# Kernel optimization log

Hardware: AMD Instinct MI355X
Metric: run time of the kernel (lower is better)

## Reference

```python
import jax, jax.numpy as jnp
import numpy as np

# Tier config (cumulative d_model [256,1024,2048], cumulative heads [4,12,24], d_k=64)
TIER_OWN = [256, 768, 1024]      # per-tier own hidden dims
HEAD_OUT = [256, 512, 768]       # n_heads_per_tier[i] * d_k
NHS = [4, 8, 12]
DKS = [64, 64, 64]
RANK = 8
IN_OFF = np.cumsum([0] + TIER_OWN)    # [0,256,1024,2048]
OUT_OFF = np.cumsum([0] + HEAD_OUT)   # [0,256,768,1536]


def _block_ut_weight(key, in_dims, out_dims):
    """Full (sum_in, sum_out) matrix with lower-triangular blocks zeroed."""
    io = np.cumsum([0] + list(in_dims))
    oo = np.cumsum([0] + list(out_dims))
    n = len(in_dims)
    mask = np.zeros((io[-1], oo[-1]), dtype=np.float32)
    for i in range(n):
        for j in range(i, n):
            mask[io[i]:io[i + 1], oo[j]:oo[j + 1]] = 1.0
    W = jax.random.normal(key, (io[-1], oo[-1]), dtype=jnp.float32) * 0.02
    return W * jnp.asarray(mask)


def setup_inputs() -> dict:
    key = jax.random.key(0)
    ks = jax.random.split(key, 16)
    B, T, D = 4, 1024, 2048
    x = jax.random.normal(ks[0], (B, T, D), dtype=jnp.float32)
    W_Q = _block_ut_weight(ks[1], TIER_OWN, HEAD_OUT)
    W_K = _block_ut_weight(ks[2], TIER_OWN, HEAD_OUT)
    W_V = _block_ut_weight(ks[3], TIER_OWN, HEAD_OUT)
    W_O = _block_ut_weight(ks[4], HEAD_OUT, TIER_OWN)
    # feedback for tiers 0 and 1 (tier 2 has no higher tiers)
    hi0 = TIER_OWN[1] + TIER_OWN[2]  # 1792
    hi1 = TIER_OWN[2]                # 1024
    FK0 = jax.random.normal(ks[5], (hi0, NHS[0] * RANK), dtype=jnp.float32) * 0.02
    PK0 = jax.random.normal(ks[6], (NHS[0], RANK, DKS[0]), dtype=jnp.float32) * 0.01
    FV0 = jax.random.normal(ks[7], (hi0, NHS[0] * RANK), dtype=jnp.float32) * 0.02
    PV0 = jax.random.normal(ks[8], (NHS[0], RANK, DKS[0]), dtype=jnp.float32) * 0.01
    FK1 = jax.random.normal(ks[9], (hi1, NHS[1] * RANK), dtype=jnp.float32) * 0.02
    PK1 = jax.random.normal(ks[10], (NHS[1], RANK, DKS[1]), dtype=jnp.float32) * 0.01
    FV1 = jax.random.normal(ks[11], (hi1, NHS[1] * RANK), dtype=jnp.float32) * 0.02
    PV1 = jax.random.normal(ks[12], (NHS[1], RANK, DKS[1]), dtype=jnp.float32) * 0.01
    return dict(x=x, W_Q=W_Q, W_K=W_K, W_V=W_V, W_O=W_O,
                FK0=FK0, PK0=PK0, FV0=FV0, PV0=PV0,
                FK1=FK1, PK1=PK1, FV1=FV1, PV1=PV1)


def _forward(x, W_Q, W_K, W_V, W_O, FK0, PK0, FV0, PV0, FK1, PK1, FV1, PV1):
    B, T, _ = x.shape
    Q_all = x @ W_Q
    K_all = x @ W_K
    V_all = x @ W_V
    causal = jnp.tril(jnp.ones((T, T), dtype=bool))
    fb = {0: (FK0, PK0, FV0, PV0), 1: (FK1, PK1, FV1, PV1)}
    head_outs = []
    for tier in range(3):
        nh, dk = NHS[tier], DKS[tier]
        dim = nh * dk
        o = int(OUT_OFF[tier])
        Q = Q_all[..., o:o + dim]
        K = K_all[..., o:o + dim]
        V = V_all[..., o:o + dim]
        if tier in fb:
            Fk, Pk, Fv, Pv = fb[tier]
            h_hi = x[..., int(IN_OFF[tier + 1]):]  # higher tiers' hidden
            c_k = (h_hi @ Fk).reshape(B, T, nh, RANK)
            K = K + jnp.einsum('bthr,hrd->bthd', c_k, Pk).reshape(B, T, dim)
            c_v = (h_hi @ Fv).reshape(B, T, nh, RANK)
            V = V + jnp.einsum('bthr,hrd->bthd', c_v, Pv).reshape(B, T, dim)
        Qh = Q.reshape(B, T, nh, dk).transpose(0, 2, 1, 3)
        Kh = K.reshape(B, T, nh, dk).transpose(0, 2, 1, 3)
        Vh = V.reshape(B, T, nh, dk).transpose(0, 2, 1, 3)
        scores = jnp.einsum('bhqd,bhkd->bhqk', Qh, Kh) / jnp.sqrt(jnp.float32(dk))
        scores = jnp.where(causal, scores, jnp.float32(-1e30))
        attn = jax.nn.softmax(scores, axis=-1)
        out = jnp.einsum('bhqk,bhkd->bhqd', attn, Vh)
        head_outs.append(out.transpose(0, 2, 1, 3).reshape(B, T, dim))
    return jnp.concatenate(head_outs, axis=-1) @ W_O


def reference(x, W_Q, W_K, W_V, W_O, FK0, PK0, FV0, PV0, FK1, PK1, FV1, PV1):
    return _forward(x, W_Q, W_K, W_V, W_O, FK0, PK0, FV0, PV0, FK1, PK1, FV1, PV1)
```

## Files before the change

kernel.cpp:

```cpp
#include <hip/hip_runtime.h>


typedef short bf16x8 __attribute__((ext_vector_type(8)));
typedef float floatx4 __attribute__((ext_vector_type(4)));

__device__ __forceinline__ unsigned short f2bf(float f) {
  unsigned u = __builtin_bit_cast(unsigned, f);
  u += 0x7fffu + ((u >> 16) & 1u);
  return (unsigned short)(u >> 16);
}

__device__ __forceinline__ void gload_lds16(const unsigned short* g, unsigned short* l) {
  __builtin_amdgcn_global_load_lds((const __attribute__((address_space(1))) unsigned int*)g,
                                   (__attribute__((address_space(3))) unsigned int*)l, 16, 0, 0);
}

__global__ __launch_bounds__(256) void k_prep(
    const float* __restrict__ x, unsigned short* __restrict__ X16,
    const float* __restrict__ WQ, const float* __restrict__ WK, const float* __restrict__ WV,
    const float* __restrict__ FK0, const float* __restrict__ PK0,
    const float* __restrict__ FV0, const float* __restrict__ PV0,
    const float* __restrict__ FK1, const float* __restrict__ PK1,
    const float* __restrict__ FV1, const float* __restrict__ PV1,
    unsigned short* __restrict__ WTQKV,
    const float* __restrict__ WO, unsigned short* __restrict__ WTO) {
  __shared__ float tile[32][33];
  __shared__ float Fs[32][9];
  __shared__ float Ps[8][32];
  const int bid = blockIdx.x;
  const int tid = threadIdx.x;
  if (bid < 8192) {
    int i = bid * 256 + tid;
    float4 v = ((const float4*)x)[i];
    union { unsigned short u[4]; uint2 v2; } o;
    o.u[0] = f2bf(v.x); o.u[1] = f2bf(v.y); o.u[2] = f2bf(v.z); o.u[3] = f2bf(v.w);
    ((uint2*)X16)[i] = o.v2;
    return;
  }
  const int tx = tid & 31, ty = tid >> 5;
  if (bid < 17408) {
    int t = bid - 8192;
    int k0 = (t & 63) * 32, n0 = (t >> 6) * 32;
    const float* src; int nboff;
    if (n0 < 1536)      { src = WQ; nboff = n0; }
    else if (n0 < 3072) { src = WK; nboff = n0 - 1536; }
    else                { src = WV; nboff = n0 - 3072; }
#pragma unroll
    for (int j = 0; j < 4; ++j) {
      int kk = ty + j * 8;
      tile[kk][tx] = src[(size_t)(k0 + kk) * 1536 + nboff + tx];
    }
    int corrsel = 0; const float* Fsrc = nullptr; const float* Psrc = nullptr;
    int h = 0, d0 = 0, fs = 0, koff = 0;
    if (n0 >= 1536) {
      bool isK = (n0 < 3072);
      int np0 = isK ? (n0 - 1536) : (n0 - 3072);
      if (np0 < 256) {
        if (k0 >= 256) { corrsel = 1; Fsrc = isK ? FK0 : FV0; Psrc = isK ? PK0 : PV0;
                         h = np0 >> 6; d0 = np0 & 63; fs = 32; koff = k0 - 256; }
      } else if (np0 < 768) {
        if (k0 >= 1024) { corrsel = 1; Fsrc = isK ? FK1 : FV1; Psrc = isK ? PK1 : PV1;
                          h = (np0 - 256) >> 6; d0 = (np0 - 256) & 63; fs = 64; koff = k0 - 1024; }
      }
    }
    if (corrsel) {
      Fs[tid >> 3][tid & 7] = Fsrc[(size_t)(koff + (tid >> 3)) * fs + h * 8 + (tid & 7)];
      Ps[tid >> 5][tid & 31] = Psrc[h * 512 + (tid >> 5) * 64 + d0 + (tid & 31)];
    }
    __syncthreads();
#pragma unroll
    for (int j = 0; j < 4; ++j) {
      int nn = ty + j * 8;
      float v = tile[tx][nn];
      if (corrsel) {
        float c = 0.f;
#pragma unroll
        for (int r = 0; r < 8; ++r) c += Fs[tx][r] * Ps[r][nn];
        v += c;
      }
      WTQKV[(size_t)(n0 + nn) * 2048 + k0 + tx] = f2bf(v);
    }
  } else {
    int t = bid - 17408;
    int k0 = (t % 48) * 32, n0 = (t / 48) * 32;
#pragma unroll
    for (int j = 0; j < 4; ++j)
      tile[ty + j * 8][tx] = WO[(size_t)(k0 + ty + j * 8) * 2048 + n0 + tx];
    __syncthreads();
#pragma unroll
    for (int j = 0; j < 4; ++j)
      WTO[(size_t)(n0 + ty + j * 8) * 1536 + k0 + tx] = f2bf(tile[tx][ty + j * 8]);
  }
}

__device__ __forceinline__ int lds_off(int row, int kq) {
  int L = row >> 1;
  return L * 64 + ((((row & 1) << 2) | kq) ^ (L & 7)) * 8;
}

__global__ __launch_bounds__(512) void k_gemm1(const unsigned short* __restrict__ A,
                                               const unsigned short* __restrict__ Bt,
                                               unsigned short* __restrict__ C) {
  __shared__ unsigned short Ls[3][2][8192];
  const int tid = threadIdx.x;
  const int wave = tid >> 6, lane = tid & 63;
  const int qd = lane >> 4, ln = lane & 15;
  const int wr = wave >> 2, wc = wave & 3;
  int idx = blockIdx.x, bx, by, Keff;
  if (idx < 240)      { bx = 3 + idx % 15; by = idx / 15; Keff = 2048; }
  else if (idx < 272) { int t2 = idx - 240; bx = 1 + (t2 & 1); by = t2 >> 1; Keff = 1024; }
  else                { bx = 0; by = idx - 272; Keff = 256; }
  const int bm = by * 256, bn = bx * 256;
  const int NT = Keff >> 5;

  const int Lr = tid >> 3, sl = tid & 7;
  const int gg = sl ^ (Lr & 7);
  const int srow = 2 * Lr + (gg >> 2);
  const int skg = gg & 3;
  const unsigned short* gA = A + (size_t)(bm + srow) * 2048 + skg * 8;
  const unsigned short* gB = Bt + (size_t)(bn + srow) * 2048 + skg * 8;

  int aoff[8], boff[4];
#pragma unroll
  for (int mi = 0; mi < 8; ++mi) aoff[mi] = lds_off(wr * 128 + mi * 16 + ln, qd);
#pragma unroll
  for (int ni = 0; ni < 4; ++ni) boff[ni] = lds_off(wc * 64 + ni * 16 + ln, qd);

  floatx4 acc[8][4];
#pragma unroll
  for (int i = 0; i < 8; ++i)
#pragma unroll
    for (int j = 0; j < 4; ++j) acc[i][j] = (floatx4){0.f, 0.f, 0.f, 0.f};

  {
    unsigned short* d = &Ls[0][0][wave * 512];
    gload_lds16(gA, d);                 gload_lds16(gA + 128 * 2048, d + 4096);
    d = &Ls[0][1][wave * 512];
    gload_lds16(gB, d);                 gload_lds16(gB + 128 * 2048, d + 4096);
    d = &Ls[1][0][wave * 512];
    gload_lds16(gA + 32, d);            gload_lds16(gA + 128 * 2048 + 32, d + 4096);
    d = &Ls[1][1][wave * 512];
    gload_lds16(gB + 32, d);            gload_lds16(gB + 128 * 2048 + 32, d + 4096);
  }
  asm volatile("s_waitcnt vmcnt(4)" ::: "memory");
  __builtin_amdgcn_s_barrier();

  int b = 0;
  for (int t = 0; t < NT; ++t) {
    const int b2 = (b >= 1) ? b - 1 : b + 2;
    const unsigned short* la = &Ls[b][0][0];
    const unsigned short* lb = &Ls[b][1][0];
    const bool pf = (t + 2) < NT;
    const int k2 = (t + 2) << 5;
    bf16x8 bfr[4], af[4];
#pragma unroll
    for (int ni = 0; ni < 4; ++ni) bfr[ni] = *(const bf16x8*)(lb + boff[ni]);
#pragma unroll
    for (int mi = 0; mi < 4; ++mi) af[mi] = *(const bf16x8*)(la + aoff[mi]);
    if (pf) {
      unsigned short* d = &Ls[b2][0][wave * 512];
      gload_lds16(gA + k2, d);
      gload_lds16(gA + 128 * 2048 + k2, d + 4096);
    }
    __builtin_amdgcn_s_barrier();
    __builtin_amdgcn_s_setprio(1);
#pragma unroll
    for (int mi = 0; mi < 4; ++mi)
#pragma unroll
      for (int ni = 0; ni < 4; ++ni)
        acc[mi][ni] = __builtin_amdgcn_mfma_f32_16x16x32_bf16(af[mi], bfr[ni], acc[mi][ni], 0, 0, 0);
    __builtin_amdgcn_s_setprio(0);
    __builtin_amdgcn_s_barrier();
#pragma unroll
    for (int mi = 0; mi < 4; ++mi) af[mi] = *(const bf16x8*)(la + aoff[4 + mi]);
    if (pf) {
      unsigned short* d = &Ls[b2][1][wave * 512];
      gload_lds16(gB + k2, d);
      gload_lds16(gB + 128 * 2048 + k2, d + 4096);
    }
    __builtin_amdgcn_s_barrier();
    __builtin_amdgcn_s_setprio(1);
#pragma unroll
    for (int mi = 0; mi < 4; ++mi)
#pragma unroll
      for (int ni = 0; ni < 4; ++ni)
        acc[4 + mi][ni] = __builtin_amdgcn_mfma_f32_16x16x32_bf16(af[mi], bfr[ni], acc[4 + mi][ni], 0, 0, 0);
    __builtin_amdgcn_s_setprio(0);
    if (t + 1 < NT) {
      if (pf) asm volatile("s_waitcnt vmcnt(4)" ::: "memory");
      else    asm volatile("s_waitcnt vmcnt(0)" ::: "memory");
      __builtin_amdgcn_s_barrier();
    }
    b = (b == 2) ? 0 : b + 1;
  }
#pragma unroll
  for (int mi = 0; mi < 8; ++mi)
#pragma unroll
    for (int r = 0; r < 4; ++r) {
      size_t row = (size_t)(bm + wr * 128 + mi * 16 + qd * 4 + r);
#pragma unroll
      for (int ni = 0; ni < 4; ++ni) {
        int col = bn + wc * 64 + ni * 16 + ln;
        C[row * 4608 + col] = f2bf(acc[mi][ni][r]);
      }
    }
}

template <bool OUT_BF16, int MODE>
__global__ __launch_bounds__(256) void k_gemm_bt(const unsigned short* __restrict__ A,
                                                 const unsigned short* __restrict__ Bt,
                                                 void* __restrict__ C, int M, int N, int K) {
  __shared__ unsigned short As[128 * 64];
  __shared__ unsigned short Bs[128 * 64];
  const int tid = threadIdx.x;
  const int wave = tid >> 6, lane = tid & 63;
  const int qd = lane >> 4, ln = lane & 15;
  int idx = blockIdx.x, bx, by;
  if (MODE == 0) {
    if (idx < 960)       { bx = 6 + idx % 30; by = idx / 30; }
    else if (idx < 1088) { int t = idx - 960; bx = 2 + (t & 3); by = t >> 2; }
    else                 { int t = idx - 1088; bx = t & 1; by = t >> 1; }
  } else {
    if (idx < 256)       { bx = 8 + (idx & 7); by = idx >> 3; }
    else if (idx < 448)  { int t = idx - 256; bx = 2 + t % 6; by = t / 6; }
    else                 { int t = idx - 448; bx = t & 1; by = t >> 1; }
  }
  const int bm = by * 128, bn = bx * 128;
  const int wr = wave >> 1, wc = wave & 1;
  int Keff;
  if (MODE == 0) Keff = (bn < 256) ? 256 : (bn < 768 ? 1024 : 2048);
  else           Keff = (bn < 256) ? 256 : (bn < 1024 ? 768 : 1536);
  floatx4 acc[4][4];
#pragma unroll
  for (int i = 0; i < 4; ++i)
#pragma unroll
    for (int j = 0; j < 4; ++j) acc[i][j] = (floatx4){0.f, 0.f, 0.f, 0.f};
  const int rl = lane >> 3;
  const int sg = (lane & 7) ^ rl;
  const unsigned short* gA = A + (size_t)(bm + wave * 32 + rl) * K + sg * 8;
  const unsigned short* gB = Bt + (size_t)(bn + wave * 32 + rl) * K + sg * 8;
  unsigned short* lA = As + wave * 2048;
  unsigned short* lB = Bs + wave * 2048;
  const int l7 = ln & 7;
  for (int k0 = 0; k0 < Keff; k0 += 64) {
    __syncthreads();
#pragma unroll
    for (int i = 0; i < 4; ++i) {
      gload_lds16(gA + (size_t)8 * i * K + k0, lA + i * 512);
      gload_lds16(gB + (size_t)8 * i * K + k0, lB + i * 512);
    }
    __syncthreads();
#pragma unroll
    for (int h = 0; h < 2; ++h) {
      bf16x8 af[4], bfr[4];
#pragma unroll
      for (int mi = 0; mi < 4; ++mi)
        af[mi] = *(const bf16x8*)(As + (wr * 64 + mi * 16 + ln) * 64 + ((h * 4 + qd) ^ l7) * 8);
#pragma unroll
      for (int ni = 0; ni < 4; ++ni)
        bfr[ni] = *(const bf16x8*)(Bs + (wc * 64 + ni * 16 + ln) * 64 + ((h * 4 + qd) ^ l7) * 8);
#pragma unroll
      for (int mi = 0; mi < 4; ++mi)
#pragma unroll
        for (int ni = 0; ni < 4; ++ni)
          acc[mi][ni] = __builtin_amdgcn_mfma_f32_16x16x32_bf16(af[mi], bfr[ni], acc[mi][ni], 0, 0, 0);
    }
  }
#pragma unroll
  for (int mi = 0; mi < 4; ++mi)
#pragma unroll
    for (int r = 0; r < 4; ++r) {
      int row = bm + wr * 64 + mi * 16 + qd * 4 + r;
#pragma unroll
      for (int ni = 0; ni < 4; ++ni) {
        int col = bn + wc * 64 + ni * 16 + ln;
        if (OUT_BF16)
          ((unsigned short*)C)[(size_t)row * N + col] = f2bf(acc[mi][ni][r]);
        else
          ((float*)C)[(size_t)row * N + col] = acc[mi][ni][r];
      }
    }
}

__global__ void k_transpose_v(const unsigned short* __restrict__ QKV,
                              unsigned short* __restrict__ VT) {
  __shared__ unsigned short t[64 * 65];
  const int tt = blockIdx.x * 64, dt = blockIdx.y * 64, b = blockIdx.z;
  const int tid = threadIdx.x;
  const int r = tid >> 3, c0 = (tid & 7) * 8;
#pragma unroll
  for (int i = 0; i < 2; ++i) {
    int tok = r + i * 32;
    union { uint4 v; unsigned short u[8]; } vv;
    vv.v = *(const uint4*)(QKV + (size_t)(b * 1024 + tt + tok) * 4608 + 3072 + dt + c0);
#pragma unroll
    for (int j = 0; j < 8; ++j) t[tok * 65 + c0 + j] = vv.u[j];
  }
  __syncthreads();
#pragma unroll
  for (int i = 0; i < 2; ++i) {
    int d = r + i * 32;
    union { uint4 v; unsigned short u[8]; } vv;
#pragma unroll
    for (int j = 0; j < 8; ++j) vv.u[j] = t[(c0 + j) * 65 + d];
    *(uint4*)(VT + ((size_t)b * 1536 + dt + d) * 1024 + tt + c0) = vv.v;
  }
}

#define LDP 136
__global__ __launch_bounds__(256) void k_attn(const unsigned short* __restrict__ QKV,
                                              const unsigned short* __restrict__ VT,
                                              unsigned short* __restrict__ Oout) {
  __shared__ unsigned short Ks[128 * 64];
  __shared__ unsigned short VTs[64 * 128];
  __shared__ unsigned short Pl[4][16 * LDP];
  const int tid = threadIdx.x;
  const int wave = tid >> 6, lane = tid & 63;
  const int qd = lane >> 4, ln = lane & 15;
  const int qb = (int)gridDim.x - 1 - (int)blockIdx.x;
  const int gh = blockIdx.y, b = blockIdx.z;
  const int T = 1024, LD = 4608;
  const size_t rowbase = (size_t)b * T * LD;
  const int qcol = 64 * gh, kcol = 1536 + 64 * gh;
  const unsigned short* VTg = VT + ((size_t)b * 1536 + 64 * gh) * 1024;
  const float SCALE = 0.18033688f;
  const int q0 = qb * 128 + wave * 16;

  bf16x8 aq[2][2];
#pragma unroll
  for (int j = 0; j < 2; ++j) {
    const unsigned short* qp = QKV + rowbase + (size_t)(q0 + j * 64 + ln) * LD + qcol;
    aq[j][0] = *(const bf16x8*)(qp + qd * 8);
    aq[j][1] = *(const bf16x8*)(qp + 32 + qd * 8);
  }
  floatx4 Oacc[2][4];
#pragma unroll
  for (int j = 0; j < 2; ++j)
#pragma unroll
    for (int i = 0; i < 4; ++i) Oacc[j][i] = (floatx4){0.f, 0.f, 0.f, 0.f};
  float l_lane[2] = {0.f, 0.f};

  const int rk = lane >> 3;
  const int gk = ((lane & 7) ^ rk) * 8;
  const unsigned short* gK = QKV + rowbase + (size_t)(wave * 32 + rk) * LD + kcol + gk;
  unsigned short* lK = Ks + wave * 32 * 64;
  const int rv = lane >> 4;
  const int cv = lane & 15;
  unsigned short* lV = VTs + wave * 16 * 128;
  const unsigned short* gVrow[4];
  int gvcol[4];
#pragma unroll
  for (int i = 0; i < 4; ++i) {
    int d = wave * 16 + 4 * i + rv;
    gVrow[i] = VTg + (size_t)d * 1024;
    gvcol[i] = (cv ^ (4 * i + rv)) * 8;
  }
  const int l7 = ln & 7;

  for (int jt = 0; jt <= qb; ++jt) {
    const int jk = jt * 128;
    const bool diag = (jt == qb);
    __syncthreads();
#pragma unroll
    for (int i = 0; i < 4; ++i) {
      gload_lds16(gK + (size_t)(jk + 8 * i) * LD, lK + i * 512);
      gload_lds16(gVrow[i] + jk + gvcol[i], lV + i * 512);
    }
    __syncthreads();

#pragma unroll
    for (int j = 0; j < 2; ++j) {
      const bool dj0 = diag && (j == 0);
      const int hmax = dj0 ? 4 : 8;
      floatx4 Sc[8];
#pragma unroll
      for (int h = 0; h < 8; ++h) {
        if (h >= hmax) continue;
        Sc[h] = (floatx4){0.f, 0.f, 0.f, 0.f};
        bf16x8 a0 = *(const bf16x8*)(Ks + (h * 16 + ln) * 64 + (qd ^ l7) * 8);
        bf16x8 a1 = *(const bf16x8*)(Ks + (h * 16 + ln) * 64 + ((4 + qd) ^ l7) * 8);
        Sc[h] = __builtin_amdgcn_mfma_f32_16x16x32_bf16(a0, aq[j][0], Sc[h], 0, 0, 0);
        Sc[h] = __builtin_amdgcn_mfma_f32_16x16x32_bf16(a1, aq[j][1], Sc[h], 0, 0, 0);
      }
      const int qrow = q0 + j * 64 + ln;
      unsigned short* pw = Pl[wave];
#pragma unroll
      for (int h = 0; h < 8; ++h) {
        if (h >= hmax) continue;
        union { unsigned short u[4]; uint2 v; } pk;
#pragma unroll
        for (int r = 0; r < 4; ++r) {
          float v = fminf(Sc[h][r] * SCALE, 80.f);
          float p = __builtin_amdgcn_exp2f(v);
          if (diag && (j == 0 || h >= 4)) {
            int key = jk + h * 16 + qd * 4 + r;
            if (key > qrow) p = 0.f;
          }
          l_lane[j] += p;
          pk.u[r] = f2bf(p);
        }
        *(uint2*)(pw + ln * LDP + h * 16 + qd * 4) = pk.v;
      }
      __asm__ volatile("s_waitcnt lgkmcnt(0)" ::: "memory");
      const int smax = dj0 ? 2 : 4;
      bf16x8 pa[4];
#pragma unroll
      for (int s = 0; s < 4; ++s) {
        if (s >= smax) continue;
        pa[s] = *(const bf16x8*)(pw + ln * LDP + s * 32 + qd * 8);
      }
#pragma unroll
      for (int nc = 0; nc < 4; ++nc) {
        const int d = nc * 16 + ln;
#pragma unroll
        for (int s = 0; s < 4; ++s) {
          if (s >= smax) continue;
          bf16x8 bv = *(const bf16x8*)(VTs + d * 128 + (((s * 4 + qd) ^ ln) & 15) * 8);
          Oacc[j][nc] = __builtin_amdgcn_mfma_f32_16x16x32_bf16(pa[s], bv, Oacc[j][nc], 0, 0, 0);
        }
      }
    }
  }
#pragma unroll
  for (int j = 0; j < 2; ++j) {
    float l = l_lane[j];
    l += __shfl_xor(l, 16, 64);
    l += __shfl_xor(l, 32, 64);
#pragma unroll
    for (int r = 0; r < 4; ++r) {
      float inv = 1.0f / __shfl(l, qd * 4 + r, 64);
      size_t row = (size_t)b * T + q0 + j * 64 + qd * 4 + r;
#pragma unroll
      for (int nc = 0; nc < 4; ++nc)
        Oout[row * 1536 + 64 * gh + nc * 16 + ln] = f2bf(Oacc[j][nc][r] * inv);
    }
  }
}

extern "C" void kernel_launch(void* const* d_in, const int* in_sizes, int n_in,
                              void* d_out, int out_size, void* d_ws, size_t ws_size,
                              hipStream_t stream) {
  (void)in_sizes; (void)n_in; (void)out_size; (void)ws_size;
  const float* x   = (const float*)d_in[0];
  const float* WQ  = (const float*)d_in[1];
  const float* WK  = (const float*)d_in[2];
  const float* WV  = (const float*)d_in[3];
  const float* WO  = (const float*)d_in[4];
  const float* FK0 = (const float*)d_in[5];
  const float* PK0 = (const float*)d_in[6];
  const float* FV0 = (const float*)d_in[7];
  const float* PV0 = (const float*)d_in[8];
  const float* FK1 = (const float*)d_in[9];
  const float* PK1 = (const float*)d_in[10];
  const float* FV1 = (const float*)d_in[11];
  const float* PV1 = (const float*)d_in[12];

  char* ws = (char*)d_ws;
  unsigned short* X16   = (unsigned short*)(ws + 0);
  unsigned short* VTb   = X16;
  unsigned short* WTQKV = (unsigned short*)(ws + 16777216);
  unsigned short* QKV   = (unsigned short*)(ws + 35651584);
  unsigned short* ATT   = (unsigned short*)(ws + 73400320);
  unsigned short* WTO   = (unsigned short*)(ws + 85983232);

  k_prep<<<20480, 256, 0, stream>>>(x, X16, WQ, WK, WV,
                                    FK0, PK0, FV0, PV0, FK1, PK1, FV1, PV1,
                                    WTQKV, WO, WTO);
  k_gemm1<<<288, 512, 0, stream>>>(X16, WTQKV, QKV);
  k_transpose_v<<<dim3(16, 24, 4), 256, 0, stream>>>(QKV, VTb);
  k_attn<<<dim3(8, 24, 4), 256, 0, stream>>>(QKV, VTb, ATT);
  k_gemm_bt<false, 1><<<512, 256, 0, stream>>>(ATT, WTO, d_out, 4096, 2048, 1536);
}
```

Baseline: 333.3 us.

## Rewrite output projection GEMM with triple-buffered async LDS pipeline and 64x128 tiles

Replaces the generic two-barrier output projection GEMM with a specialised kernel that uses 64x128 tiles (1024 blocks), K-steps of 32, and a three-stage LDS ring fed by direct global-to-LDS loads, with vmcnt waits so loads overlap MFMA work. It also raises wave priority around the MFMA bursts and keeps the block-upper-triangular K skipping via a per-block tile count. The aim is to hide load latency and raise occupancy and parallelism for the 4096x2048x1536 GEMM, at the cost of smaller per-wave tiles and heavier reliance on hand-tuned waitcnt correctness. The kernel depends on an lds_off helper that must already exist elsewhere in the file.

```diff
diff --git a/kernel.cpp b/kernel.cpp
--- a/kernel.cpp
+++ b/kernel.cpp
@@ -206,78 +206,95 @@
     }
 }
 
-template <bool OUT_BF16, int MODE>
-__global__ __launch_bounds__(256) void k_gemm_bt(const unsigned short* __restrict__ A,
-                                                 const unsigned short* __restrict__ Bt,
-                                                 void* __restrict__ C, int M, int N, int K) {
-  __shared__ unsigned short As[128 * 64];
-  __shared__ unsigned short Bs[128 * 64];
+#define G2_VM3 asm volatile("s_waitcnt vmcnt(3)" ::: "memory")
+#define G2_VM0 asm volatile("s_waitcnt vmcnt(0)" ::: "memory")
+
+#define G2_STEP(AP, BP, AQ, BQ, STG, K2, FINQ)                                  \
+  do {                                                                          \
+    bf16x8 af[4], bfr[2];                                                       \
+    _Pragma("unroll")                                                           \
+    for (int mi = 0; mi < 4; ++mi) af[mi] = *(const bf16x8*)((AP) + aoff[mi]);  \
+    _Pragma("unroll")                                                           \
+    for (int ni = 0; ni < 2; ++ni) bfr[ni] = *(const bf16x8*)((BP) + boff[ni]); \
+    if (STG) {                                                                  \
+      gload_lds16(gAs + (K2), (AQ) + wave * 512);                               \
+      gload_lds16(gBs + (K2), (BQ) + wave * 512);                               \
+      gload_lds16(gBs + 64 * 1536 + (K2), (BQ) + 2048 + wave * 512);            \
+    }                                                                           \
+    __builtin_amdgcn_s_barrier();                                               \
+    __builtin_amdgcn_s_setprio(1);                                              \
+    _Pragma("unroll")                                                           \
+    for (int mi = 0; mi < 4; ++mi)                                              \
+      _Pragma("unroll")                                                         \
+      for (int ni = 0; ni < 2; ++ni)                                            \
+        acc[mi][ni] = __builtin_amdgcn_mfma_f32_16x16x32_bf16(af[mi], bfr[ni], acc[mi][ni], 0, 0, 0); \
+    __builtin_amdgcn_s_setprio(0);                                              \
+    if (FINQ) {                                                                 \
+      if (STG) { G2_VM3; } else { G2_VM0; }                                     \
+      __builtin_amdgcn_s_barrier();                                             \
+    }                                                                           \
+  } while (0)
+
+__global__ __launch_bounds__(256) void k_gemm2(const unsigned short* __restrict__ A,
+                                               const unsigned short* __restrict__ Bt,
+                                               float* __restrict__ C) {
+  __shared__ unsigned short As0[2048], As1[2048], As2[2048];
+  __shared__ unsigned short Bs0[4096], Bs1[4096], Bs2[4096];
   const int tid = threadIdx.x;
   const int wave = tid >> 6, lane = tid & 63;
   const int qd = lane >> 4, ln = lane & 15;
-  int idx = blockIdx.x, bx, by;
-  if (MODE == 0) {
-    if (idx < 960)       { bx = 6 + idx % 30; by = idx / 30; }
-    else if (idx < 1088) { int t = idx - 960; bx = 2 + (t & 3); by = t >> 2; }
-    else                 { int t = idx - 1088; bx = t & 1; by = t >> 1; }
-  } else {
-    if (idx < 256)       { bx = 8 + (idx & 7); by = idx >> 3; }
-    else if (idx < 448)  { int t = idx - 256; bx = 2 + t % 6; by = t / 6; }
-    else                 { int t = idx - 448; bx = t & 1; by = t >> 1; }
-  }
-  const int bm = by * 128, bn = bx * 128;
-  const int wr = wave >> 1, wc = wave & 1;
-  int Keff;
-  if (MODE == 0) Keff = (bn < 256) ? 256 : (bn < 768 ? 1024 : 2048);
-  else           Keff = (bn < 256) ? 256 : (bn < 1024 ? 768 : 1536);
-  floatx4 acc[4][4];
+  const int idx = blockIdx.x;
+  int bx, by, NT;
+  if (idx < 512)      { bx = 8 + (idx >> 6); by = idx & 63; NT = 48; }
+  else if (idx < 896) { int t = idx - 512; bx = 2 + (t >> 6); by = t & 63; NT = 24; }
+  else                { int t = idx - 896; bx = t >> 6; by = t & 63; NT = 9; }
+  const int bm = by * 64, bn = bx * 128;
+
+  const int Lr = tid >> 3, sl = tid & 7;
+  const int gg = sl ^ (Lr & 7);
+  const int srow = 2 * Lr + (gg >> 2);
+  const int skg = gg & 3;
+  const unsigned short* gAs = A + (size_t)(bm + srow) * 1536 + skg * 8;
+  const unsigned short* gBs = Bt + (size_t)(bn + srow) * 1536 + skg * 8;
+
+  int aoff[4], boff[2];
+#pragma unroll
+  for (int mi = 0; mi < 4; ++mi) aoff[mi] = lds_off(mi * 16 + ln, qd);
+#pragma unroll
+  for (int ni = 0; ni < 2; ++ni) boff[ni] = lds_off(wave * 32 + ni * 16 + ln, qd);
+
+  floatx4 acc[4][2];
 #pragma unroll
   for (int i = 0; i < 4; ++i)
 #pragma unroll
-    for (int j = 0; j < 4; ++j) acc[i][j] = (floatx4){0.f, 0.f, 0.f, 0.f};
-  const int rl = lane >> 3;
-  const int sg = (lane & 7) ^ rl;
-  const unsigned short* gA = A + (size_t)(bm + wave * 32 + rl) * K + sg * 8;
-  const unsigned short* gB = Bt + (size_t)(bn + wave * 32 + rl) * K + sg * 8;
-  unsigned short* lA = As + wave * 2048;
-  unsigned short* lB = Bs + wave * 2048;
-  const int l7 = ln & 7;
-  for (int k0 = 0; k0 < Keff; k0 += 64) {
-    __syncthreads();
-#pragma unroll
-    for (int i = 0; i < 4; ++i) {
-      gload_lds16(gA + (size_t)8 * i * K + k0, lA + i * 512);
-      gload_lds16(gB + (size_t)8 * i * K + k0, lB + i * 512);
-    }
-    __syncthreads();
-#pragma unroll
-    for (int h = 0; h < 2; ++h) {
-      bf16x8 af[4], bfr[4];
-#pragma unroll
-      for (int mi = 0; mi < 4; ++mi)
-        af[mi] = *(const bf16x8*)(As + (wr * 64 + mi * 16 + ln) * 64 + ((h * 4 + qd) ^ l7) * 8);
-#pragma unroll
-      for (int ni = 0; ni < 4; ++ni)
-        bfr[ni] = *(const bf16x8*)(Bs + (wc * 64 + ni * 16 + ln) * 64 + ((h * 4 + qd) ^ l7) * 8);
-#pragma unroll
-      for (int mi = 0; mi < 4; ++mi)
-#pragma unroll
-        for (int ni = 0; ni < 4; ++ni)
-          acc[mi][ni] = __builtin_amdgcn_mfma_f32_16x16x32_bf16(af[mi], bfr[ni], acc[mi][ni], 0, 0, 0);
-    }
-  }
+    for (int j = 0; j < 2; ++j) acc[i][j] = (floatx4){0.f, 0.f, 0.f, 0.f};
+
+  gload_lds16(gAs, As0 + wave * 512);
+  gload_lds16(gBs, Bs0 + wave * 512);
+  gload_lds16(gBs + 64 * 1536, Bs0 + 2048 + wave * 512);
+  gload_lds16(gAs + 32, As1 + wave * 512);
+  gload_lds16(gBs + 32, Bs1 + wave * 512);
+  gload_lds16(gBs + 64 * 1536 + 32, Bs1 + 2048 + wave * 512);
+  G2_VM3;
+  __builtin_amdgcn_s_barrier();
+
+  const int NT3 = NT / 3;
+  for (int i = 0; i < NT3; ++i) {
+    const int t0 = 3 * i;
+    G2_STEP(As0, Bs0, As2, Bs2, (t0 + 2) < NT, (t0 + 2) * 32, (t0 + 1) < NT);
+    G2_STEP(As1, Bs1, As0, Bs0, (t0 + 3) < NT, (t0 + 3) * 32, (t0 + 2) < NT);
+    G2_STEP(As2, Bs2, As1, Bs1, (t0 + 4) < NT, (t0 + 4) * 32, (t0 + 3) < NT);
+  }
+
 #pragma unroll
   for (int mi = 0; mi < 4; ++mi)
 #pragma unroll
     for (int r = 0; r < 4; ++r) {
-      int row = bm + wr * 64 + mi * 16 + qd * 4 + r;
-#pragma unroll
-      for (int ni = 0; ni < 4; ++ni) {
-        int col = bn + wc * 64 + ni * 16 + ln;
-        if (OUT_BF16)
-          ((unsigned short*)C)[(size_t)row * N + col] = f2bf(acc[mi][ni][r]);
-        else
-          ((float*)C)[(size_t)row * N + col] = acc[mi][ni][r];
+      size_t row = (size_t)(bm + mi * 16 + qd * 4 + r);
+#pragma unroll
+      for (int ni = 0; ni < 2; ++ni) {
+        int col = bn + wave * 32 + ni * 16 + ln;
+        C[row * 2048 + col] = acc[mi][ni][r];
       }
     }
 }
@@ -469,5 +486,5 @@
   k_gemm1<<<288, 512, 0, stream>>>(X16, WTQKV, QKV);
   k_transpose_v<<<dim3(16, 24, 4), 256, 0, stream>>>(QKV, VTb);
   k_attn<<<dim3(8, 24, 4), 256, 0, stream>>>(QKV, VTb, ATT);
-  k_gemm_bt<false, 1><<<512, 256, 0, stream>>>(ATT, WTO, d_out, 4096, 2048, 1536);
-}
+  k_gemm2<<<1024, 256, 0, stream>>>(ATT, WTO, (float*)d_out);
+}
```

After: 335.2 us. No clear change (+0.6%).
